# Performance work log

Measured on AMD Instinct MI355X. Metric: run time of the kernel, lower is better.

The kernel has to match this reference:

```python
import jax, jax.numpy as jnp
import numpy as np

C = 128      # in_channels == out_channels
K = 3        # kernel_size
PAD = 1
DIL = 1
EPS = 1e-5


def setup_inputs() -> dict:
    key = jax.random.key(0)
    ks = jax.random.split(key, 6)
    B, L = 8, 16384
    x = jax.random.normal(ks[0], (B, C, L), jnp.float32)
    # depthwise Conv1d(C, C, K, groups=C), bias=True (nn.Conv1d default)
    dw_w = jax.random.normal(ks[1], (C, 1, K), jnp.float32) * (1.0 / np.sqrt(K))
    dw_b = jax.random.normal(ks[2], (C,), jnp.float32) * 0.05
    # LayerNorm(C)
    ln_g = jnp.ones((C,), jnp.float32)
    ln_b = jnp.zeros((C,), jnp.float32)
    # offset Linear(C -> groups*K) ; weight stored [out, in] like torch
    off_w = jax.random.normal(ks[3], (K, C), jnp.float32) * 0.02
    off_b = jnp.zeros((K,), jnp.float32)
    # deformable conv weight [C_out, C_in, K], bias=False
    dc_w = jax.random.normal(ks[4], (C, C, K), jnp.float32) * (1.0 / np.sqrt(C * K))
    return dict(x=x, dw_w=dw_w, dw_b=dw_b, ln_g=ln_g, ln_b=ln_b,
                off_w=off_w, off_b=off_b, dc_w=dc_w)


def _forward(x, dw_w, dw_b, ln_g, ln_b, off_w, off_b, dc_w):
    B, _, L = x.shape
    # --- dw_conv: depthwise conv + LayerNorm(channel) + ReLU ---
    y = jax.lax.conv_general_dilated(
        x, dw_w, window_strides=(1,), padding=[(PAD, PAD)],
        dimension_numbers=('NCH', 'OIH', 'NCH'), feature_group_count=C)
    y = y + dw_b[None, :, None]
    yt = y.transpose(0, 2, 1)                      # [B, L, C]
    mu = jnp.mean(yt, axis=-1, keepdims=True)
    var = jnp.mean((yt - mu) ** 2, axis=-1, keepdims=True)
    yn = (yt - mu) * jax.lax.rsqrt(var + EPS) * ln_g + ln_b
    yr = jax.nn.relu(yn)                           # [B, L, C]
    # --- offset linear: [B, L, C] -> [B, L, K] ---
    offset = yr @ off_w.T + off_b                  # [B, L, K]
    # --- deformable conv1d with linear interpolation, zero padding ---
    base = (jnp.arange(L, dtype=x.dtype)[None, :, None]
            + (jnp.arange(K, dtype=x.dtype) * DIL - PAD)[None, None, :])
    pos = base + offset                            # [B, L, K] fractional positions
    p0 = jnp.floor(pos)
    frac = pos - p0                                # [B, L, K]
    p0i = p0.astype(jnp.int32)
    p1i = p0i + 1
    v0 = ((p0i >= 0) & (p0i < L)).astype(x.dtype)
    v1 = ((p1i >= 0) & (p1i < L)).astype(x.dtype)
    i0 = jnp.clip(p0i, 0, L - 1)
    i1 = jnp.clip(p1i, 0, L - 1)
    gather = jax.vmap(lambda xb, ib: xb[:, ib])    # xb [C,L], ib [L,K] -> [C,L,K]
    g0 = gather(x, i0)                             # [B, C, L, K]
    g1 = gather(x, i1)
    g = g0 * ((1.0 - frac) * v0)[:, None] + g1 * (frac * v1)[:, None]
    # weighted sum over input channels and kernel taps
    return jnp.einsum('bclk,ock->bol', g, dc_w)    # [B, C_out, L]


def reference(x, dw_w, dw_b, ln_g, ln_b, off_w, off_b, dc_w):
    return _forward(x, dw_w, dw_b, ln_g, ln_b, off_w, off_b, dc_w)
```

## Files before the change

kernel.cpp:

```cpp
#include <hip/hip_runtime.h>
#include <hip/hip_bf16.h>
#include <cstdint>
#include <cstddef>

#define C_CH 128
#define L_LEN 16384
#define B_N 8
#define K_T 3
#define EPS 1e-5f
#define WPAD 8
#define WIN_G 144
#define WIN_O 132

typedef __attribute__((ext_vector_type(8))) short short8;
typedef __attribute__((ext_vector_type(4))) float float4v;

__device__ __forceinline__ short f2bf(float f) {
  union { float f; unsigned u; } v; v.f = f;
  unsigned r = v.u + 0x7fffu + ((v.u >> 16) & 1u);
  return (short)(r >> 16);
}
__device__ __forceinline__ float bflo(unsigned d) {
  union { unsigned u; float f; } v; v.u = d << 16; return v.f;
}
__device__ __forceinline__ float bfhi(unsigned d) {
  union { unsigned u; float f; } v; v.u = d & 0xffff0000u; return v.f;
}
__device__ __forceinline__ unsigned packbf(float a, float b) {
  unsigned ua = __float_as_uint(a) + 0x8000u;
  unsigned ub = __float_as_uint(b) + 0x8000u;
  return (ua >> 16) | (ub & 0xffff0000u);
}
__device__ __forceinline__ int clampL(int v) {
  return v < 0 ? 0 : (v > L_LEN - 1 ? L_LEN - 1 : v);
}
__device__ __forceinline__ void gl_lds16(const void* g, void* l) {
  __builtin_amdgcn_global_load_lds(
      (const __attribute__((address_space(1))) unsigned*)g,
      (__attribute__((address_space(3))) unsigned*)l, 16, 0, 0);
}

__global__ void repack_w2(const float* __restrict__ dc_w, short* __restrict__ Wp2) {
  int tid = blockIdx.x * 256 + threadIdx.x;
  if (tid >= C_CH * C_CH * K_T) return;
  int j = tid & 7;
  int m = (tid >> 3) & 127;
  int qk = (tid >> 10) & 3;
  int ks = tid >> 12;
  int kt = ks >> 2, s = ks & 3;
  int c = qk * 32 + s * 8 + j;
  Wp2[tid] = f2bf(dc_w[(m * C_CH + c) * K_T + kt]);
}

__global__ __launch_bounds__(256, 4) void offsets_k4(
    const float* __restrict__ x,
    const float* __restrict__ dw_w, const float* __restrict__ dw_b,
    const float* __restrict__ ln_g, const float* __restrict__ ln_b,
    const float* __restrict__ off_w, const float* __restrict__ off_b,
    short* __restrict__ xT, unsigned* __restrict__ d_wab, unsigned* __restrict__ d_idx) {
  __shared__ short xs[WIN_O * 128];
  __shared__ float swt[1152];

  int t = threadIdx.x;
  int b = blockIdx.y;
  int l0 = blockIdx.x * 128;
  const float* xb = x + (size_t)b * C_CH * L_LEN;
  char* xsb = (char*)xs;

  for (int i = t; i < 1152; i += 256) {
    float v;
    if (i < 384) v = dw_w[i];
    else if (i < 512) v = dw_b[i - 384];
    else if (i < 640) v = ln_g[i - 512];
    else if (i < 768) v = ln_b[i - 640];
    else v = off_w[i - 768];
    swt[i] = v;
  }

  int lane = t & 63, wv = t >> 6;

  {
    int cc = wv * 4 + (lane >> 4);
    int lqi = lane & 15;
    #pragma unroll
    for (int i = 0; i < 3; ++i) {
      int lq = i * 16 + lqi;
      if (lq < 33) {
        int bl = l0 - 2 + lq * 4;
        float fv[8][4];
        if (bl >= 0 && bl + 3 <= L_LEN - 1) {
          #pragma unroll
          for (int j = 0; j < 8; ++j) {
            float4 f = *(const float4*)(xb + (size_t)(cc * 8 + j) * L_LEN + bl);
            fv[j][0] = f.x; fv[j][1] = f.y; fv[j][2] = f.z; fv[j][3] = f.w;
          }
        } else {
          #pragma unroll
          for (int j = 0; j < 8; ++j)
            #pragma unroll
            for (int k = 0; k < 4; ++k)
              fv[j][k] = xb[(size_t)(cc * 8 + j) * L_LEN + clampL(bl + k)];
        }
        #pragma unroll
        for (int k = 0; k < 4; ++k) {
          int rr = lq * 4 + k;
          uint4 q;
          q.x = packbf(fv[0][k], fv[1][k]);
          q.y = packbf(fv[2][k], fv[3][k]);
          q.z = packbf(fv[4][k], fv[5][k]);
          q.w = packbf(fv[6][k], fv[7][k]);
          *(uint4*)(xsb + rr * 256 + ((cc ^ (rr & 15)) << 4)) = q;
        }
      }
    }
  }
  __syncthreads();

  {
    short* xTb = xT + (size_t)b * L_LEN * C_CH;
    int sg = lane & 15;
    int rbase = wv * 4 + (lane >> 4);
    #pragma unroll
    for (int i = 0; i < 8; ++i) {
      int lr = rbase + i * 16;
      int r = lr + 2;
      uint4 q = *(const uint4*)(xsb + r * 256 + ((sg ^ (r & 15)) << 4));
      *(uint4*)(xTb + (size_t)(l0 + lr) * C_CH + sg * 8) = q;
    }
  }

  #pragma unroll
  for (int it = 0; it < 2; ++it) {
    int l_loc = (t >> 2) + it * 64;
    int sub = t & 3;
    int lg = l0 + l_loc;
    float mL = (lg >= 1) ? 1.f : 0.f;
    float mR = (lg + 1 < L_LEN) ? 1.f : 0.f;
    int rm = l_loc + 2;

    float ys[32];
    float sum = 0.f, sumsq = 0.f;
    #pragma unroll
    for (int oct = 0; oct < 4; ++oct) {
      int ch = sub * 4 + oct;
      int r0 = rm - 1, r1 = rm, r2 = rm + 1;
      uint4 q0 = *(const uint4*)(xsb + r0 * 256 + ((ch ^ (r0 & 15)) << 4));
      uint4 q1 = *(const uint4*)(xsb + r1 * 256 + ((ch ^ (r1 & 15)) << 4));
      uint4 q2 = *(const uint4*)(xsb + r2 * 256 + ((ch ^ (r2 & 15)) << 4));
      const unsigned* u0 = (const unsigned*)&q0;
      const unsigned* u1 = (const unsigned*)&q1;
      const unsigned* u2 = (const unsigned*)&q2;
      #pragma unroll
      for (int j = 0; j < 4; ++j) {
        int c = ch * 8 + 2 * j;
        float y0 = swt[384 + c] + mL * bflo(u0[j]) * swt[3 * c]
                 + bflo(u1[j]) * swt[3 * c + 1] + mR * bflo(u2[j]) * swt[3 * c + 2];
        float y1 = swt[385 + c] + mL * bfhi(u0[j]) * swt[3 * c + 3]
                 + bfhi(u1[j]) * swt[3 * c + 4] + mR * bfhi(u2[j]) * swt[3 * c + 5];
        ys[oct * 8 + 2 * j] = y0;
        ys[oct * 8 + 2 * j + 1] = y1;
        sum += y0 + y1;
        sumsq += y0 * y0 + y1 * y1;
      }
    }
    sum += __shfl_xor(sum, 1, 64);     sum += __shfl_xor(sum, 2, 64);
    sumsq += __shfl_xor(sumsq, 1, 64); sumsq += __shfl_xor(sumsq, 2, 64);
    float mean = sum * (1.f / C_CH);
    float var = sumsq * (1.f / C_CH) - mean * mean;
    float rstd = rsqrtf(var + EPS);

    float o0 = 0.f, o1 = 0.f, o2 = 0.f;
    #pragma unroll
    for (int li = 0; li < 32; ++li) {
      int c = sub * 32 + li;
      float yn = (ys[li] - mean) * rstd * swt[512 + c] + swt[640 + c];
      float yr = yn > 0.f ? yn : 0.f;
      o0 += yr * swt[768 + c];
      o1 += yr * swt[896 + c];
      o2 += yr * swt[1024 + c];
    }
    o0 += __shfl_xor(o0, 1, 64); o0 += __shfl_xor(o0, 2, 64);
    o1 += __shfl_xor(o1, 1, 64); o1 += __shfl_xor(o1, 2, 64);
    o2 += __shfl_xor(o2, 1, 64); o2 += __shfl_xor(o2, 2, 64);

    if (sub < 3) {
      float o = (sub == 0 ? o0 : (sub == 1 ? o1 : o2)) + off_b[sub];
      float pos = (float)(lg + sub - 1) + o;
      float p0f = floorf(pos);
      float fr = pos - p0f;
      int i0 = (int)p0f, i1 = i0 + 1;
      float wa = (i0 >= 0 && i0 < L_LEN) ? (1.f - fr) : 0.f;
      float wbv = (i1 >= 0 && i1 < L_LEN) ? fr : 0.f;
      int i0c = clampL(i0), i1c = clampL(i1);
      size_t di = ((size_t)b * K_T + sub) * L_LEN + lg;
      d_wab[di] = packbf(wa, wbv);
      d_idx[di] = (unsigned)i0c | ((unsigned)i1c << 16);
    }
  }
}

__global__ __launch_bounds__(256, 4) void deform_gemm3(
    const short* __restrict__ xT,
    const unsigned* __restrict__ d_wab, const unsigned* __restrict__ d_idx,
    const short* __restrict__ Wp2, float* __restrict__ out) {
  __shared__ short xs[WIN_G * 128];
  __shared__ unsigned s_wab[K_T][128];
  __shared__ unsigned s_r01[K_T][128];

  int t = threadIdx.x;
  int b = blockIdx.y;
  int l0 = blockIdx.x * 128;
  int wb0 = l0 - WPAD;
  int lane = t & 63, wv = t >> 6;
  int qk = lane >> 4, hrow = lane & 15;

  const short* xTb = xT + (size_t)b * L_LEN * C_CH;
  #pragma unroll
  for (int i = 0; i < 9; ++i) {
    int rb = wv * 36 + i * 4;
    int r = rb + (lane >> 4);
    int lrow = clampL(wb0 + r);
    int slot = lane & 15;
    const short* g = xTb + (size_t)lrow * C_CH + ((slot ^ (r & 15)) << 3);
    gl_lds16(g, &xs[rb * 128]);
  }

  for (int d = t; d < 384; d += 256) {
    int n = d & 127, tap = d >> 7;
    size_t di = ((size_t)b * K_T + tap) * L_LEN + (l0 + n);
    unsigned wab = d_wab[di];
    unsigned ii = d_idx[di];
    int r0 = (int)(ii & 0xffffu) - wb0;
    int r1 = (int)(ii >> 16) - wb0;
    if ((unsigned)r0 >= WIN_G) { r0 = 0; wab &= 0xffff0000u; }
    if ((unsigned)r1 >= WIN_G) { r1 = 0; wab &= 0x0000ffffu; }
    s_wab[tap][n] = wab;
    s_r01[tap][n] = (unsigned)r0 | ((unsigned)r1 << 16);
  }
  __syncthreads();

  float4v acc[8][2];
  #pragma unroll
  for (int i = 0; i < 8; ++i) {
    acc[i][0] = (float4v){0.f, 0.f, 0.f, 0.f};
    acc[i][1] = (float4v){0.f, 0.f, 0.f, 0.f};
  }
  const short* wpb = Wp2 + qk * 1024 + hrow * 8;
  const char* xsb = (const char*)xs;

  #pragma unroll
  for (int kt = 0; kt < 3; ++kt) {
    float wa[2], wbv[2];
    int b0[2], m0_[2], b1[2], m1_[2];
    #pragma unroll
    for (int nt = 0; nt < 2; ++nt) {
      int n = wv * 32 + nt * 16 + hrow;
      unsigned wab = s_wab[kt][n];
      wa[nt] = bflo(wab);
      wbv[nt] = bfhi(wab);
      unsigned r01 = s_r01[kt][n];
      int r0 = r01 & 0xffff, r1 = r01 >> 16;
      b0[nt] = r0 * 256; m0_[nt] = r0 & 15;
      b1[nt] = r1 * 256; m1_[nt] = r1 & 15;
    }
    #pragma unroll
    for (int s = 0; s < 4; ++s) {
      int ks = kt * 4 + s;
      int ch = qk * 4 + s;
      short8 bfrag[2];
      #pragma unroll
      for (int nt = 0; nt < 2; ++nt) {
        uint4 q0 = *(const uint4*)(xsb + b0[nt] + ((ch ^ m0_[nt]) << 4));
        uint4 q1 = *(const uint4*)(xsb + b1[nt] + ((ch ^ m1_[nt]) << 4));
        const unsigned* q0u = (const unsigned*)&q0;
        const unsigned* q1u = (const unsigned*)&q1;
        union { unsigned u[4]; short8 s8; } bu;
        #pragma unroll
        for (int j = 0; j < 4; ++j) {
          float glo = wa[nt] * bflo(q0u[j]) + wbv[nt] * bflo(q1u[j]);
          float ghi = wa[nt] * bfhi(q0u[j]) + wbv[nt] * bfhi(q1u[j]);
          bu.u[j] = packbf(glo, ghi);
        }
        bfrag[nt] = bu.s8;
      }
      const short* wk = wpb + ks * 4096;
      #pragma unroll
      for (int mt = 0; mt < 8; ++mt) {
        short8 a = *(const short8*)(wk + mt * 128);
        acc[mt][0] = __builtin_amdgcn_mfma_f32_16x16x32_bf16(a, bfrag[0], acc[mt][0], 0, 0, 0);
        acc[mt][1] = __builtin_amdgcn_mfma_f32_16x16x32_bf16(a, bfrag[1], acc[mt][1], 0, 0, 0);
      }
    }
  }

  float* ob = out + (size_t)b * C_CH * L_LEN + l0;
  #pragma unroll
  for (int mt = 0; mt < 8; ++mt) {
    #pragma unroll
    for (int nt = 0; nt < 2; ++nt) {
      int col = wv * 32 + nt * 16 + hrow;
      #pragma unroll
      for (int r = 0; r < 4; ++r) {
        ob[(size_t)(mt * 16 + qk * 4 + r) * L_LEN + col] = acc[mt][nt][r];
      }
    }
  }
}

extern "C" void kernel_launch(void* const* d_in, const int* in_sizes, int n_in,
                              void* d_out, int out_size, void* d_ws, size_t ws_size,
                              hipStream_t stream) {
  const float* x    = (const float*)d_in[0];
  const float* dw_w = (const float*)d_in[1];
  const float* dw_b = (const float*)d_in[2];
  const float* ln_g = (const float*)d_in[3];
  const float* ln_b = (const float*)d_in[4];
  const float* off_w = (const float*)d_in[5];
  const float* off_b = (const float*)d_in[6];
  const float* dc_w = (const float*)d_in[7];
  float* out = (float*)d_out;

  char* ws = (char*)d_ws;
  short* xT = (short*)ws;
  short* Wp2 = (short*)(ws + 0x2000000);
  unsigned* d_wab = (unsigned*)(ws + 0x2018000);
  unsigned* d_idx = (unsigned*)(ws + 0x2198000);

  hipLaunchKernelGGL(repack_w2, dim3(192), dim3(256), 0, stream, dc_w, Wp2);
  hipLaunchKernelGGL(offsets_k4, dim3(L_LEN / 128, B_N), dim3(256), 0, stream,
                     x, dw_w, dw_b, ln_g, ln_b, off_w, off_b, xT, d_wab, d_idx);
  hipLaunchKernelGGL(deform_gemm3, dim3(L_LEN / 128, B_N), dim3(256), 0, stream,
                     xT, d_wab, d_idx, Wp2, out);
}
```

Before: 190.3 us.

## Fuse offset computation and deformable GEMM into one kernel sharing the LDS window

```diff
diff --git a/kernel.cpp b/kernel.cpp
--- a/kernel.cpp
+++ b/kernel.cpp
@@ -8,9 +8,8 @@
 #define B_N 8
 #define K_T 3
 #define EPS 1e-5f
-#define WPAD 8
-#define WIN_G 144
-#define WIN_O 132
+#define WPADL 8
+#define WIN 144
 
 typedef __attribute__((ext_vector_type(8))) short short8;
 typedef __attribute__((ext_vector_type(4))) float float4v;
@@ -33,11 +32,6 @@
 }
 __device__ __forceinline__ int clampL(int v) {
   return v < 0 ? 0 : (v > L_LEN - 1 ? L_LEN - 1 : v);
-}
-__device__ __forceinline__ void gl_lds16(const void* g, void* l) {
-  __builtin_amdgcn_global_load_lds(
-      (const __attribute__((address_space(1))) unsigned*)g,
-      (__attribute__((address_space(3))) unsigned*)l, 16, 0, 0);
 }
 
 __global__ void repack_w2(const float* __restrict__ dc_w, short* __restrict__ Wp2) {
@@ -52,28 +46,30 @@
   Wp2[tid] = f2bf(dc_w[(m * C_CH + c) * K_T + kt]);
 }
 
-__global__ __launch_bounds__(256, 4) void offsets_k4(
+__global__ __launch_bounds__(256, 3) void fused_deform(
     const float* __restrict__ x,
     const float* __restrict__ dw_w, const float* __restrict__ dw_b,
     const float* __restrict__ ln_g, const float* __restrict__ ln_b,
     const float* __restrict__ off_w, const float* __restrict__ off_b,
-    short* __restrict__ xT, unsigned* __restrict__ d_wab, unsigned* __restrict__ d_idx) {
-  __shared__ short xs[WIN_O * 128];
-  __shared__ float swt[1152];
+    const short* __restrict__ Wp2, float* __restrict__ out) {
+  __shared__ short xs[WIN * 128];
+  __shared__ float swt[1024];
+  __shared__ unsigned s_wab[K_T][128];
+  __shared__ unsigned s_r01[K_T][128];
 
   int t = threadIdx.x;
   int b = blockIdx.y;
   int l0 = blockIdx.x * 128;
+  int wb0 = l0 - WPADL;
   const float* xb = x + (size_t)b * C_CH * L_LEN;
   char* xsb = (char*)xs;
 
-  for (int i = t; i < 1152; i += 256) {
+  for (int i = t; i < 1024; i += 256) {
     float v;
     if (i < 384) v = dw_w[i];
     else if (i < 512) v = dw_b[i - 384];
-    else if (i < 640) v = ln_g[i - 512];
-    else if (i < 768) v = ln_b[i - 640];
-    else v = off_w[i - 768];
+    else if (i < 640) v = __uint_as_float(packbf(ln_g[i - 512], ln_b[i - 512]));
+    else v = off_w[i - 640];
     swt[i] = v;
   }
 
@@ -85,8 +81,8 @@
     #pragma unroll
     for (int i = 0; i < 3; ++i) {
       int lq = i * 16 + lqi;
-      if (lq < 33) {
-        int bl = l0 - 2 + lq * 4;
+      if (lq < 36) {
+        int bl = wb0 + lq * 4;
         float fv[8][4];
         if (bl >= 0 && bl + 3 <= L_LEN - 1) {
           #pragma unroll
@@ -116,19 +112,6 @@
   }
   __syncthreads();
 
-  {
-    short* xTb = xT + (size_t)b * L_LEN * C_CH;
-    int sg = lane & 15;
-    int rbase = wv * 4 + (lane >> 4);
-    #pragma unroll
-    for (int i = 0; i < 8; ++i) {
-      int lr = rbase + i * 16;
-      int r = lr + 2;
-      uint4 q = *(const uint4*)(xsb + r * 256 + ((sg ^ (r & 15)) << 4));
-      *(uint4*)(xTb + (size_t)(l0 + lr) * C_CH + sg * 8) = q;
-    }
-  }
-
   #pragma unroll
   for (int it = 0; it < 2; ++it) {
     int l_loc = (t >> 2) + it * 64;
@@ -136,7 +119,7 @@
     int lg = l0 + l_loc;
     float mL = (lg >= 1) ? 1.f : 0.f;
     float mR = (lg + 1 < L_LEN) ? 1.f : 0.f;
-    int rm = l_loc + 2;
+    int rm = l_loc + WPADL;
 
     float ys[32];
     float sum = 0.f, sumsq = 0.f;
@@ -170,14 +153,16 @@
     float rstd = rsqrtf(var + EPS);
 
     float o0 = 0.f, o1 = 0.f, o2 = 0.f;
+    const unsigned* lngb = (const unsigned*)swt;
     #pragma unroll
     for (int li = 0; li < 32; ++li) {
       int c = sub * 32 + li;
-      float yn = (ys[li] - mean) * rstd * swt[512 + c] + swt[640 + c];
+      unsigned gb = lngb[512 + c];
+      float yn = (ys[li] - mean) * rstd * bflo(gb) + bfhi(gb);
       float yr = yn > 0.f ? yn : 0.f;
-      o0 += yr * swt[768 + c];
-      o1 += yr * swt[896 + c];
-      o2 += yr * swt[1024 + c];
+      o0 += yr * swt[640 + c];
+      o1 += yr * swt[768 + c];
+      o2 += yr * swt[896 + c];
     }
     o0 += __shfl_xor(o0, 1, 64); o0 += __shfl_xor(o0, 2, 64);
     o1 += __shfl_xor(o1, 1, 64); o1 += __shfl_xor(o1, 2, 64);
@@ -192,53 +177,18 @@
       float wa = (i0 >= 0 && i0 < L_LEN) ? (1.f - fr) : 0.f;
       float wbv = (i1 >= 0 && i1 < L_LEN) ? fr : 0.f;
       int i0c = clampL(i0), i1c = clampL(i1);
-      size_t di = ((size_t)b * K_T + sub) * L_LEN + lg;
-      d_wab[di] = packbf(wa, wbv);
-      d_idx[di] = (unsigned)i0c | ((unsigned)i1c << 16);
-    }
-  }
-}
-
-__global__ __launch_bounds__(256, 4) void deform_gemm3(
-    const short* __restrict__ xT,
-    const unsigned* __restrict__ d_wab, const unsigned* __restrict__ d_idx,
-    const short* __restrict__ Wp2, float* __restrict__ out) {
-  __shared__ short xs[WIN_G * 128];
-  __shared__ unsigned s_wab[K_T][128];
-  __shared__ unsigned s_r01[K_T][128];
-
-  int t = threadIdx.x;
-  int b = blockIdx.y;
-  int l0 = blockIdx.x * 128;
-  int wb0 = l0 - WPAD;
-  int lane = t & 63, wv = t >> 6;
+      unsigned wab = packbf(wa, wbv);
+      int r0 = i0c - wb0;
+      int r1 = i1c - wb0;
+      if ((unsigned)r0 >= WIN) { r0 = 0; wab &= 0xffff0000u; }
+      if ((unsigned)r1 >= WIN) { r1 = 0; wab &= 0x0000ffffu; }
+      s_wab[sub][l_loc] = wab;
+      s_r01[sub][l_loc] = (unsigned)r0 | ((unsigned)r1 << 16);
+    }
+  }
+  __syncthreads();
+
   int qk = lane >> 4, hrow = lane & 15;
-
-  const short* xTb = xT + (size_t)b * L_LEN * C_CH;
-  #pragma unroll
-  for (int i = 0; i < 9; ++i) {
-    int rb = wv * 36 + i * 4;
-    int r = rb + (lane >> 4);
-    int lrow = clampL(wb0 + r);
-    int slot = lane & 15;
-    const short* g = xTb + (size_t)lrow * C_CH + ((slot ^ (r & 15)) << 3);
-    gl_lds16(g, &xs[rb * 128]);
-  }
-
-  for (int d = t; d < 384; d += 256) {
-    int n = d & 127, tap = d >> 7;
-    size_t di = ((size_t)b * K_T + tap) * L_LEN + (l0 + n);
-    unsigned wab = d_wab[di];
-    unsigned ii = d_idx[di];
-    int r0 = (int)(ii & 0xffffu) - wb0;
-    int r1 = (int)(ii >> 16) - wb0;
-    if ((unsigned)r0 >= WIN_G) { r0 = 0; wab &= 0xffff0000u; }
-    if ((unsigned)r1 >= WIN_G) { r1 = 0; wab &= 0x0000ffffu; }
-    s_wab[tap][n] = wab;
-    s_r01[tap][n] = (unsigned)r0 | ((unsigned)r1 << 16);
-  }
-  __syncthreads();
-
   float4v acc[8][2];
   #pragma unroll
   for (int i = 0; i < 8; ++i) {
@@ -246,7 +196,6 @@
     acc[i][1] = (float4v){0.f, 0.f, 0.f, 0.f};
   }
   const short* wpb = Wp2 + qk * 1024 + hrow * 8;
-  const char* xsb = (const char*)xs;
 
   #pragma unroll
   for (int kt = 0; kt < 3; ++kt) {
@@ -320,15 +269,9 @@
   const float* dc_w = (const float*)d_in[7];
   float* out = (float*)d_out;
 
-  char* ws = (char*)d_ws;
-  short* xT = (short*)ws;
-  short* Wp2 = (short*)(ws + 0x2000000);
-  unsigned* d_wab = (unsigned*)(ws + 0x2018000);
-  unsigned* d_idx = (unsigned*)(ws + 0x2198000);
+  short* Wp2 = (short*)d_ws;
 
   hipLaunchKernelGGL(repack_w2, dim3(192), dim3(256), 0, stream, dc_w, Wp2);
-  hipLaunchKernelGGL(offsets_k4, dim3(L_LEN / 128, B_N), dim3(256), 0, stream,
-                     x, dw_w, dw_b, ln_g, ln_b, off_w, off_b, xT, d_wab, d_idx);
-  hipLaunchKernelGGL(deform_gemm3, dim3(L_LEN / 128, B_N), dim3(256), 0, stream,
-                     xT, d_wab, d_idx, Wp2, out);
-}
+  hipLaunchKernelGGL(fused_deform, dim3(L_LEN / 128, B_N), dim3(256), 0, stream,
+                     x, dw_w, dw_b, ln_g, ln_b, off_w, off_b, Wp2, out);
+}
```

New measurement: 190.4 us. No clear change (+0.0%).
